# Optimization experiments

Hardware: AMD Instinct MI355X
Metric: run time of the kernel (lower is better)

The kernel has to match this reference:

```python
import jax, jax.numpy as jnp
import numpy as np

B, L, D, H = 4, 2048, 2048, 16
HD = D // H
EPS = 1e-6


def _rope_tables(l, hd, base=10000.0):
    inv = 1.0 / (base ** (np.arange(0, hd, 2, dtype=np.float32) / hd))  # [hd/2]
    t = np.arange(l, dtype=np.float32)
    ang = np.outer(t, inv)  # [l, hd/2]
    return jnp.asarray(np.cos(ang)), jnp.asarray(np.sin(ang))


def setup_inputs() -> dict:
    key = jax.random.key(0)
    ks = jax.random.split(key, 8)
    cos, sin = _rope_tables(L, HD)
    s = 1.0 / np.sqrt(D)
    return {
        "x": jax.random.normal(ks[0], (B, L, D), jnp.float32),
        "freqs_cos": cos,
        "freqs_sin": sin,
        "Wqk": jax.random.normal(ks[1], (D, 2 * D), jnp.float32) * s,
        "Wv": jax.random.normal(ks[2], (D, D), jnp.float32) * s,
        "bv": jax.random.normal(ks[3], (D,), jnp.float32) * 0.02,
        "Wp": jax.random.normal(ks[4], (D, D), jnp.float32) * s,
        "bp": jax.random.normal(ks[5], (D,), jnp.float32) * 0.02,
        "qn_w": jnp.ones((HD,), jnp.float32),
        "kn_w": jnp.ones((HD,), jnp.float32),
    }


def _rmsnorm(x, w, eps=EPS):
    ms = jnp.mean(jnp.square(x), axis=-1, keepdims=True)
    return x * jax.lax.rsqrt(ms + eps) * w


def _rope(x, cos, sin):
    # x: [b,h,l,hd]; cos/sin: [l,hd/2]; interleaved (complex) rotation
    x1 = x[..., 0::2]
    x2 = x[..., 1::2]
    c = cos[None, None, :, :]
    s = sin[None, None, :, :]
    out = jnp.stack([x1 * c - x2 * s, x1 * s + x2 * c], axis=-1)
    return out.reshape(x.shape)


def reference(x, freqs_cos, freqs_sin, Wqk, Wv, bv, Wp, bp, qn_w, kn_w):
    b, l, d = x.shape
    qk = x @ Wqk  # [b,l,2d]
    q, k = jnp.split(qk, 2, axis=-1)
    v = x @ Wv + bv
    # [b,l,d] -> [b,h,l,hd]
    to_heads = lambda t: t.reshape(b, l, H, HD).transpose(0, 2, 1, 3)
    q, k, v = to_heads(q), to_heads(k), to_heads(v)
    q = _rmsnorm(q, qn_w)
    k = _rmsnorm(k, kn_w)
    q = _rope(q, freqs_cos, freqs_sin)
    k = _rope(k, freqs_cos, freqs_sin)
    scale = 1.0 / jnp.sqrt(jnp.asarray(HD, q.dtype))
    scores = jnp.einsum("bhqd,bhkd->bhqk", q, k) * scale
    causal = jnp.tril(jnp.ones((l, l), bool))
    scores = jnp.where(causal[None, None], scores, jnp.asarray(-1e30, scores.dtype))
    attn = jax.nn.softmax(scores, axis=-1)
    y = jnp.einsum("bhqk,bhkd->bhqd", attn, v)
    y = y.transpose(0, 2, 1, 3).reshape(b, l, d)
    return y @ Wp + bp
```

## Files before the change

### kernel.cpp

```cpp
#include <hip/hip_runtime.h>
#include <hip/hip_bf16.h>
#include <math.h>

#define B_  4
#define L_  2048
#define D_  2048
#define H_  16
#define HD_ 128
#define BH_ (B_*H_)
#define BL_ (B_*L_)

typedef __attribute__((ext_vector_type(4))) float  f32x4;
typedef __attribute__((ext_vector_type(8))) __bf16 bf16x8;

static __device__ __forceinline__ float bf2f(unsigned short u) {
    union { unsigned int i; float f; } v; v.i = ((unsigned int)u) << 16; return v.f;
}
static __device__ __forceinline__ unsigned short f2bf(float f) {
    union { float f; unsigned int i; } v; v.f = f;
    unsigned int x = v.i;
    return (unsigned short)((x + 0x7fffu + ((x >> 16) & 1u)) >> 16);
}

static __device__ __forceinline__ void gload16(const unsigned short* g, unsigned short* l) {
    __builtin_amdgcn_global_load_lds(
        (const __attribute__((address_space(1))) unsigned int*)(const void*)g,
        (__attribute__((address_space(3))) unsigned int*)(void*)l, 16, 0, 0);
}

__global__ __launch_bounds__(256) void k_f32_to_bf16(const float* __restrict__ s,
                                                     unsigned short* __restrict__ d, int n8) {
    int i = blockIdx.x * 256 + threadIdx.x;
    if (i >= n8) return;
    const float* p = s + (size_t)i * 8;
    float4 a = *(const float4*)p;
    float4 b = *(const float4*)(p + 4);
    union { bf16x8 v; unsigned short u[8]; } o;
    o.u[0]=f2bf(a.x); o.u[1]=f2bf(a.y); o.u[2]=f2bf(a.z); o.u[3]=f2bf(a.w);
    o.u[4]=f2bf(b.x); o.u[5]=f2bf(b.y); o.u[6]=f2bf(b.z); o.u[7]=f2bf(b.w);
    *(bf16x8*)(d + (size_t)i * 8) = o.v;
}

__global__ __launch_bounds__(256) void k_transpose_f2b(const float* __restrict__ src,
                                                       unsigned short* __restrict__ dst,
                                                       int R, int C, int dstStride) {
    __shared__ float tile[32][33];
    int tx = threadIdx.x & 31, ty = threadIdx.x >> 5;
    int c0 = blockIdx.x * 32, r0 = blockIdx.y * 32;
    #pragma unroll
    for (int i = 0; i < 32; i += 8)
        tile[ty + i][tx] = src[(size_t)(r0 + ty + i) * C + c0 + tx];
    __syncthreads();
    #pragma unroll
    for (int i = 0; i < 32; i += 8)
        dst[(size_t)(c0 + ty + i) * dstStride + r0 + tx] = f2bf(tile[tx][ty + i]);
}


template<int MG, int NG>
static __device__ __forceinline__ void mfma_quad(const bf16x8 (&afr)[4][2],
                                                 const bf16x8 (&bfr)[2][2],
                                                 f32x4 (&acc)[8][4]) {
    #pragma unroll
    for (int mi = 0; mi < 4; ++mi)
        #pragma unroll
        for (int ni = 0; ni < 2; ++ni) {
            acc[MG*4+mi][NG*2+ni] = __builtin_amdgcn_mfma_f32_16x16x32_bf16(
                afr[mi][0], bfr[ni][0], acc[MG*4+mi][NG*2+ni], 0, 0, 0);
            acc[MG*4+mi][NG*2+ni] = __builtin_amdgcn_mfma_f32_16x16x32_bf16(
                afr[mi][1], bfr[ni][1], acc[MG*4+mi][NG*2+ni], 0, 0, 0);
        }
}

static __device__ __forceinline__ void ds_load_a(const unsigned short* u, int wm,
                                                 int l15, int l4, bf16x8 (&afr)[4][2]) {
    int sw = l15 & 7;
    #pragma unroll
    for (int mi = 0; mi < 4; ++mi) {
        int ro = (wm*64 + mi*16 + l15) * 64;
        afr[mi][0] = *(const bf16x8*)(u + ro + ((l4 ^ sw) << 3));
        afr[mi][1] = *(const bf16x8*)(u + ro + (((4 + l4) ^ sw) << 3));
    }
}

static __device__ __forceinline__ void ds_load_b(const unsigned short* u, int wn,
                                                 int l15, int l4, bf16x8 (&bfr)[2][2]) {
    int sw = l15 & 7;
    #pragma unroll
    for (int ni = 0; ni < 2; ++ni) {
        int ro = (wn*32 + ni*16 + l15) * 64;
        bfr[ni][0] = *(const bf16x8*)(u + ro + ((l4 ^ sw) << 3));
        bfr[ni][1] = *(const bf16x8*)(u + ro + (((4 + l4) ^ sw) << 3));
    }
}

#define STAGE_A_(c_, mg_, t_) do {                                                        \
    gload16(gA + (size_t)(((mg_)*64      ) * 2048) + (t_)*64, &Lds[c_][0][mg_][w*512]);   \
    gload16(gA + (size_t)(((mg_)*64 + 128) * 2048) + (t_)*64, &Lds[c_][0][mg_][4096 + w*512]); \
} while (0)
#define STAGE_B_(c_, ng_, t_) do {                                                        \
    gload16(gB + (size_t)(((ng_)*32 + ((w>>2)    )*64) * 2048) + (t_)*64, &Lds[c_][1][ng_][w*512]); \
    gload16(gB + (size_t)(((ng_)*32 + ((w>>2) + 2)*64) * 2048) + (t_)*64, &Lds[c_][1][ng_][4096 + w*512]); \
} while (0)
#define SB_() __builtin_amdgcn_sched_barrier(0)
#define READS_(c_) do {                                              \
    ds_load_a(&Lds[c_][0][0][0], wm, l15, l4, afr);  SB_();          \
    ds_load_b(&Lds[c_][1][0][0], wn, l15, l4, bf0);  SB_();          \
    ds_load_b(&Lds[c_][1][1][0], wn, l15, l4, bf1);  SB_();          \
    ds_load_a(&Lds[c_][0][1][0], wm, l15, l4, afr2); SB_();          \
} while (0)

template<int MODE>
__global__ __launch_bounds__(512, 2) void k_gemm(const unsigned short* __restrict__ A,
                                                 const unsigned short* __restrict__ Bt,
                                                 int M, int N, int K,
                                                 const float* __restrict__ bias,
                                                 unsigned short* __restrict__ qout,
                                                 unsigned short* __restrict__ kout,
                                                 unsigned short* __restrict__ vout,
                                                 float* __restrict__ fout) {
    (void)K;
    __shared__ __align__(16) unsigned short Lds[2][2][2][8192];
    const int tid = threadIdx.x;
    const int lane = tid & 63, w = tid >> 6;
    const int wm = w >> 2, wn = w & 3;
    const int l15 = lane & 15, l4 = lane >> 4;
    const int lsw = (lane & 7) ^ ((lane >> 3) & 7);

    int nwgx = gridDim.x;
    int bid = blockIdx.y * nwgx + blockIdx.x;
    int cpx = (nwgx * gridDim.y) >> 3;
    int sb = (bid & 7) * cpx + (bid >> 3);
    int n0 = (sb % nwgx) * 256, m0 = (sb / nwgx) * 256;

    const unsigned short* gA = A  + (size_t)(m0 + w*8 + (lane >> 3)) * 2048 + lsw*8;
    const unsigned short* gB = Bt + (size_t)(n0 + (w&3)*8 + (lane >> 3)) * 2048 + lsw*8;

    f32x4 acc[8][4] = {};
    bf16x8 afr[4][2], afr2[4][2], bf0[2][2], bf1[2][2];
    const int nt = 2048 / 64;

    STAGE_A_(0, 0, 0); STAGE_B_(0, 0, 0); STAGE_B_(0, 1, 0); STAGE_A_(0, 1, 0);
    STAGE_A_(1, 0, 1); STAGE_B_(1, 0, 1); STAGE_B_(1, 1, 1);
    asm volatile("s_waitcnt vmcnt(6)" ::: "memory");
    __builtin_amdgcn_s_barrier();
    READS_(0);

    for (int t = 0; t < nt; ++t) {
        const int c = t & 1, cn = c ^ 1;
        const bool h1 = (t + 1 < nt), h2 = (t + 2 < nt);

        if (h1) STAGE_A_(cn, 1, t + 1);
        __builtin_amdgcn_s_barrier();
        asm volatile("s_waitcnt lgkmcnt(12)" ::: "memory");
        SB_();
        __builtin_amdgcn_s_setprio(1);
        mfma_quad<0, 0>(afr, bf0, acc);
        __builtin_amdgcn_s_setprio(0);
        SB_();
        __builtin_amdgcn_s_barrier();

        if (h2) STAGE_A_(c, 0, t + 2);
        asm volatile("s_waitcnt lgkmcnt(8)" ::: "memory");
        SB_();
        __builtin_amdgcn_s_setprio(1);
        mfma_quad<0, 1>(afr, bf1, acc);
        __builtin_amdgcn_s_setprio(0);
        SB_();
        __builtin_amdgcn_s_barrier();

        if (h2) { STAGE_B_(c, 0, t + 2); STAGE_B_(c, 1, t + 2); }
        asm volatile("s_waitcnt lgkmcnt(0)" ::: "memory");
        SB_();
        __builtin_amdgcn_s_setprio(1);
        mfma_quad<1, 1>(afr2, bf1, acc);
        mfma_quad<1, 0>(afr2, bf0, acc);
        __builtin_amdgcn_s_setprio(0);
        SB_();
        if (h2) asm volatile("s_waitcnt vmcnt(6)" ::: "memory");
        else    asm volatile("s_waitcnt vmcnt(0)" ::: "memory");
        SB_();
        if (h1) READS_(cn);
        __builtin_amdgcn_s_barrier();
    }

    #pragma unroll
    for (int mi = 0; mi < 8; ++mi) {
        #pragma unroll
        for (int ni = 0; ni < 4; ++ni) {
            int ncol = n0 + wn*64 + ni*16 + l15;
            int mbase = m0 + wm*128 + mi*16 + l4*4;
            if (MODE == 0 && ncol >= 4096) {
                int cc = ncol - 4096, h = cc >> 7, hd = cc & 127;
                int b = mbase >> 11, l = mbase & 2047;
                float bv = bias[cc];
                ushort4 o;
                o.x = f2bf(acc[mi][ni][0] + bv);
                o.y = f2bf(acc[mi][ni][1] + bv);
                o.z = f2bf(acc[mi][ni][2] + bv);
                o.w = f2bf(acc[mi][ni][3] + bv);
                *(ushort4*)(vout + ((size_t)((b*H_ + h) * HD_ + hd)) * L_ + l) = o;
            } else {
                #pragma unroll
                for (int j = 0; j < 4; ++j) {
                    int m = mbase + j;
                    float v = acc[mi][ni][j];
                    if (MODE == 0) {
                        int b = m >> 11, l = m & 2047;
                        if (ncol < 2048) {
                            int h = ncol >> 7, hd = ncol & 127;
                            qout[((size_t)(b*H_ + h) * L_ + l) * HD_ + hd] = f2bf(v);
                        } else {
                            int cc = ncol - 2048, h = cc >> 7, hd = cc & 127;
                            kout[((size_t)(b*H_ + h) * L_ + l) * HD_ + hd] = f2bf(v);
                        }
                    } else {
                        fout[(size_t)m * N + ncol] = v + bias[ncol];
                    }
                }
            }
        }
    }
}

__global__ __launch_bounds__(256) void k_normrope(unsigned short* __restrict__ qb,
                                                  unsigned short* __restrict__ kb,
                                                  const float* __restrict__ cosT,
                                                  const float* __restrict__ sinT,
                                                  const float* __restrict__ qw,
                                                  const float* __restrict__ kw) {
    const float QSCL = 0.08838834764831845f * 1.4426950408889634f;
    int lane = threadIdx.x & 63;
    int row = blockIdx.x * 4 + (threadIdx.x >> 6);
    int isK = row >= BH_ * L_;
    unsigned short* buf = isK ? kb : qb;
    const float* w = isK ? kw : qw;
    int r = isK ? row - BH_ * L_ : row;
    int l = r & (L_ - 1);
    unsigned short* p = buf + (size_t)r * HD_ + lane * 2;
    ushort2 u = *(const ushort2*)p;
    float x1 = bf2f(u.x), x2 = bf2f(u.y);
    float ss = x1*x1 + x2*x2;
    #pragma unroll
    for (int off = 32; off; off >>= 1) ss += __shfl_xor(ss, off);
    float rs = rsqrtf(ss * (1.0f / 128.0f) + 1e-6f);
    rs *= isK ? 1.0f : QSCL;
    float c = cosT[l * 64 + lane], s = sinT[l * 64 + lane];
    float y1 = x1 * rs * w[lane * 2];
    float y2 = x2 * rs * w[lane * 2 + 1];
    ushort2 o;
    o.x = f2bf(y1 * c - y2 * s);
    o.y = f2bf(y1 * s + y2 * c);
    *(ushort2*)p = o;
}

#define PLDT 72

__global__ __launch_bounds__(256) void k_attn(const unsigned short* __restrict__ qbuf,
                                              const unsigned short* __restrict__ kbuf,
                                              const unsigned short* __restrict__ vT,
                                              unsigned short* __restrict__ yb) {
    __shared__ __align__(16) unsigned short Ks[64 * 128];
    __shared__ __align__(16) unsigned short Vs[128 * 64];
    __shared__ __align__(16) unsigned short Ps[4][32 * PLDT];
    int tid = threadIdx.x, lane = tid & 63, w = tid >> 6;
    int l15 = lane & 15, l4 = lane >> 4;
    int qb = 15 - (blockIdx.x >> 6);
    int bh = blockIdx.x & 63;
    const unsigned short* Q  = qbuf + (size_t)bh * L_ * HD_;
    const unsigned short* Kp = kbuf + (size_t)bh * L_ * HD_;
    const unsigned short* Vp = vT   + (size_t)bh * L_ * HD_;
    int qr0 = qb * 128 + w * 32;

    bf16x8 qf[2][4];
    #pragma unroll
    for (int m = 0; m < 2; ++m)
        #pragma unroll
        for (int ks = 0; ks < 4; ++ks)
            qf[m][ks] = *(const bf16x8*)(Q + (size_t)(qr0 + m*16 + l15) * HD_ + ks*32 + l4*8);

    f32x4 accO[2][8] = {};
    f32x4 accW[2] = {};

    bf16x8 vones;
    #pragma unroll
    for (int i = 0; i < 8; ++i) vones[i] = (__bf16)1.0f;

    const float BOUND = 20.0f;
    int nkt = 2 * qb + 2;

    for (int kt = 0; kt < nkt; ++kt) {
        int kbase = kt * 64;
        #pragma unroll
        for (int i = 0; i < 4; ++i) {
            int g = w * 4 + i;
            int kr = g * 4 + (lane >> 4);
            gload16(Kp + (size_t)(kbase + kr) * HD_ + (((lane & 15) ^ (kr & 15)) << 3),
                    Ks + g * 512);
            int vr = g * 8 + (lane >> 3);
            gload16(Vp + (size_t)vr * L_ + kbase + (((lane & 7) ^ (vr & 7)) << 3),
                    Vs + g * 512);
        }
        __syncthreads();

        if (kbase <= qr0 + 31) {
            f32x4 sf[2][4] = {};
            __builtin_amdgcn_s_setprio(1);
            #pragma unroll
            for (int f = 0; f < 4; ++f)
                #pragma unroll
                for (int ks = 0; ks < 4; ++ks) {
                    bf16x8 kf = *(const bf16x8*)(Ks + (f*16 + l15) * 128 +
                                                 ((((ks*4) + l4) ^ l15) << 3));
                    sf[0][f] = __builtin_amdgcn_mfma_f32_16x16x32_bf16(qf[0][ks], kf, sf[0][f], 0, 0, 0);
                    sf[1][f] = __builtin_amdgcn_mfma_f32_16x16x32_bf16(qf[1][ks], kf, sf[1][f], 0, 0, 0);
                }
            __builtin_amdgcn_s_setprio(0);

            unsigned short* ps = Ps[w];
            #pragma unroll
            for (int m = 0; m < 2; ++m) {
                bool needmask = (kbase + 63 > qr0 + m*16);
                #pragma unroll
                for (int f = 0; f < 4; ++f)
                    #pragma unroll
                    for (int j = 0; j < 4; ++j) {
                        float s = sf[m][f][j];
                        if (needmask) {
                            int key  = kbase + f*16 + l15;
                            int qrow = qr0 + m*16 + l4*4 + j;
                            if (key > qrow) s = -1e30f;
                        }
                        float p = exp2f(s - BOUND);
                        *(__bf16*)(ps + (m*16 + l4*4 + j) * PLDT + f*16 + l15) = (__bf16)p;
                    }
            }

            __builtin_amdgcn_s_setprio(1);
            #pragma unroll
            for (int ks = 0; ks < 2; ++ks) {
                bf16x8 pa0 = *(const bf16x8*)(ps + l15 * PLDT + ks*32 + l4*8);
                bf16x8 pa1 = *(const bf16x8*)(ps + (16 + l15) * PLDT + ks*32 + l4*8);
                #pragma unroll
                for (int cf = 0; cf < 8; ++cf) {
                    bf16x8 vf = *(const bf16x8*)(Vs + (cf*16 + l15) * 64 +
                                                 ((((ks*4) + l4) ^ (l15 & 7)) << 3));
                    accO[0][cf] = __builtin_amdgcn_mfma_f32_16x16x32_bf16(pa0, vf, accO[0][cf], 0, 0, 0);
                    accO[1][cf] = __builtin_amdgcn_mfma_f32_16x16x32_bf16(pa1, vf, accO[1][cf], 0, 0, 0);
                }
                accW[0] = __builtin_amdgcn_mfma_f32_16x16x32_bf16(pa0, vones, accW[0], 0, 0, 0);
                accW[1] = __builtin_amdgcn_mfma_f32_16x16x32_bf16(pa1, vones, accW[1], 0, 0, 0);
            }
            __builtin_amdgcn_s_setprio(0);
        }
        __syncthreads();
    }

    int b = bh >> 4, h = bh & 15;
    #pragma unroll
    for (int m = 0; m < 2; ++m)
        #pragma unroll
        for (int cf = 0; cf < 8; ++cf)
            #pragma unroll
            for (int j = 0; j < 4; ++j) {
                int qrow = qr0 + m*16 + l4*4 + j;
                float o = accO[m][cf][j] / accW[m][j];
                yb[((size_t)(b * L_ + qrow)) * D_ + h*128 + cf*16 + l15] = f2bf(o);
            }
}

extern "C" void kernel_launch(void* const* d_in, const int* in_sizes, int n_in,
                              void* d_out, int out_size, void* d_ws, size_t ws_size,
                              hipStream_t stream) {
    const float* x    = (const float*)d_in[0];
    const float* fcos = (const float*)d_in[1];
    const float* fsin = (const float*)d_in[2];
    const float* Wqk  = (const float*)d_in[3];
    const float* Wv   = (const float*)d_in[4];
    const float* bv   = (const float*)d_in[5];
    const float* Wp   = (const float*)d_in[6];
    const float* bp   = (const float*)d_in[7];
    const float* qn_w = (const float*)d_in[8];
    const float* kn_w = (const float*)d_in[9];
    float* out = (float*)d_out;

    char* ws = (char*)d_ws;
    unsigned short* Wt   = (unsigned short*)(ws);
    unsigned short* Wpt  = (unsigned short*)(ws + 25165824);
    unsigned short* xb   = (unsigned short*)(ws + 33554432);
    unsigned short* qbuf = (unsigned short*)(ws + 67108864);
    unsigned short* kbuf = (unsigned short*)(ws + 100663296);
    unsigned short* vTb  = (unsigned short*)(ws + 167772160);
    unsigned short* yb   = xb;

    k_f32_to_bf16<<<8192, 256, 0, stream>>>(x, xb, BL_ * D_ / 8);
    k_transpose_f2b<<<dim3(128, 64), 256, 0, stream>>>(Wqk, Wt, 2048, 4096, 2048);
    k_transpose_f2b<<<dim3(64, 64),  256, 0, stream>>>(Wv,  Wt + (size_t)4096 * 2048, 2048, 2048, 2048);
    k_transpose_f2b<<<dim3(64, 64),  256, 0, stream>>>(Wp,  Wpt, 2048, 2048, 2048);

    k_gemm<0><<<dim3(24, 32), 512, 0, stream>>>(xb, Wt, BL_, 6144, 2048, bv,
                                                qbuf, kbuf, vTb, nullptr);
    k_normrope<<<2 * BH_ * L_ / 4, 256, 0, stream>>>(qbuf, kbuf, fcos, fsin, qn_w, kn_w);
    k_attn<<<BH_ * (L_ / 128), 256, 0, stream>>>(qbuf, kbuf, vTb, yb);
    k_gemm<1><<<dim3(8, 32), 512, 0, stream>>>(yb, Wpt, BL_, 2048, 2048, bp,
                                               nullptr, nullptr, nullptr, out);
}
```

Before: 453.3 us.

## Shrink GEMM tiles to 128x128 with 4 waves and simpler double-buffered pipeline

```diff
diff --git a/kernel.cpp b/kernel.cpp
--- a/kernel.cpp
+++ b/kernel.cpp
@@ -57,61 +57,31 @@
 }
 
 
-template<int MG, int NG>
-static __device__ __forceinline__ void mfma_quad(const bf16x8 (&afr)[4][2],
-                                                 const bf16x8 (&bfr)[2][2],
-                                                 f32x4 (&acc)[8][4]) {
-    #pragma unroll
-    for (int mi = 0; mi < 4; ++mi)
-        #pragma unroll
-        for (int ni = 0; ni < 2; ++ni) {
-            acc[MG*4+mi][NG*2+ni] = __builtin_amdgcn_mfma_f32_16x16x32_bf16(
-                afr[mi][0], bfr[ni][0], acc[MG*4+mi][NG*2+ni], 0, 0, 0);
-            acc[MG*4+mi][NG*2+ni] = __builtin_amdgcn_mfma_f32_16x16x32_bf16(
-                afr[mi][1], bfr[ni][1], acc[MG*4+mi][NG*2+ni], 0, 0, 0);
-        }
-}
-
-static __device__ __forceinline__ void ds_load_a(const unsigned short* u, int wm,
-                                                 int l15, int l4, bf16x8 (&afr)[4][2]) {
+static __device__ __forceinline__ void ds_load4(const unsigned short* u, int half,
+                                                int l15, int l4, bf16x8 (&fr)[4][2]) {
     int sw = l15 & 7;
     #pragma unroll
-    for (int mi = 0; mi < 4; ++mi) {
-        int ro = (wm*64 + mi*16 + l15) * 64;
-        afr[mi][0] = *(const bf16x8*)(u + ro + ((l4 ^ sw) << 3));
-        afr[mi][1] = *(const bf16x8*)(u + ro + (((4 + l4) ^ sw) << 3));
+    for (int i = 0; i < 4; ++i) {
+        int ro = (half*64 + i*16 + l15) * 64;
+        fr[i][0] = *(const bf16x8*)(u + ro + ((l4 ^ sw) << 3));
+        fr[i][1] = *(const bf16x8*)(u + ro + (((4 + l4) ^ sw) << 3));
     }
 }
 
-static __device__ __forceinline__ void ds_load_b(const unsigned short* u, int wn,
-                                                 int l15, int l4, bf16x8 (&bfr)[2][2]) {
-    int sw = l15 & 7;
-    #pragma unroll
-    for (int ni = 0; ni < 2; ++ni) {
-        int ro = (wn*32 + ni*16 + l15) * 64;
-        bfr[ni][0] = *(const bf16x8*)(u + ro + ((l4 ^ sw) << 3));
-        bfr[ni][1] = *(const bf16x8*)(u + ro + (((4 + l4) ^ sw) << 3));
-    }
-}
-
-#define STAGE_A_(c_, mg_, t_) do {                                                        \
-    gload16(gA + (size_t)(((mg_)*64      ) * 2048) + (t_)*64, &Lds[c_][0][mg_][w*512]);   \
-    gload16(gA + (size_t)(((mg_)*64 + 128) * 2048) + (t_)*64, &Lds[c_][0][mg_][4096 + w*512]); \
+#define SB_() __builtin_amdgcn_sched_barrier(0)
+#define STAGE_T_(c_, t_) do {                                                         \
+    gload16(gA + (size_t)(0*32) * 2048 + (t_)*64, &Lds[c_][0][0*2048 + w*512]);       \
+    gload16(gB + (size_t)(0*32) * 2048 + (t_)*64, &Lds[c_][1][0*2048 + w*512]);       \
+    gload16(gA + (size_t)(1*32) * 2048 + (t_)*64, &Lds[c_][0][1*2048 + w*512]);       \
+    gload16(gB + (size_t)(1*32) * 2048 + (t_)*64, &Lds[c_][1][1*2048 + w*512]);       \
+    gload16(gA + (size_t)(2*32) * 2048 + (t_)*64, &Lds[c_][0][2*2048 + w*512]);       \
+    gload16(gB + (size_t)(2*32) * 2048 + (t_)*64, &Lds[c_][1][2*2048 + w*512]);       \
+    gload16(gA + (size_t)(3*32) * 2048 + (t_)*64, &Lds[c_][0][3*2048 + w*512]);       \
+    gload16(gB + (size_t)(3*32) * 2048 + (t_)*64, &Lds[c_][1][3*2048 + w*512]);       \
 } while (0)
-#define STAGE_B_(c_, ng_, t_) do {                                                        \
-    gload16(gB + (size_t)(((ng_)*32 + ((w>>2)    )*64) * 2048) + (t_)*64, &Lds[c_][1][ng_][w*512]); \
-    gload16(gB + (size_t)(((ng_)*32 + ((w>>2) + 2)*64) * 2048) + (t_)*64, &Lds[c_][1][ng_][4096 + w*512]); \
-} while (0)
-#define SB_() __builtin_amdgcn_sched_barrier(0)
-#define READS_(c_) do {                                              \
-    ds_load_a(&Lds[c_][0][0][0], wm, l15, l4, afr);  SB_();          \
-    ds_load_b(&Lds[c_][1][0][0], wn, l15, l4, bf0);  SB_();          \
-    ds_load_b(&Lds[c_][1][1][0], wn, l15, l4, bf1);  SB_();          \
-    ds_load_a(&Lds[c_][0][1][0], wm, l15, l4, afr2); SB_();          \
-} while (0)
 
 template<int MODE>
-__global__ __launch_bounds__(512, 2) void k_gemm(const unsigned short* __restrict__ A,
+__global__ __launch_bounds__(256, 2) void k_gemm(const unsigned short* __restrict__ A,
                                                  const unsigned short* __restrict__ Bt,
                                                  int M, int N, int K,
                                                  const float* __restrict__ bias,
@@ -120,10 +90,10 @@
                                                  unsigned short* __restrict__ vout,
                                                  float* __restrict__ fout) {
     (void)K;
-    __shared__ __align__(16) unsigned short Lds[2][2][2][8192];
+    __shared__ __align__(16) unsigned short Lds[2][2][8192];
     const int tid = threadIdx.x;
     const int lane = tid & 63, w = tid >> 6;
-    const int wm = w >> 2, wn = w & 3;
+    const int wm = w >> 1, wn = w & 1;
     const int l15 = lane & 15, l4 = lane >> 4;
     const int lsw = (lane & 7) ^ ((lane >> 3) & 7);
 
@@ -131,65 +101,59 @@
     int bid = blockIdx.y * nwgx + blockIdx.x;
     int cpx = (nwgx * gridDim.y) >> 3;
     int sb = (bid & 7) * cpx + (bid >> 3);
-    int n0 = (sb % nwgx) * 256, m0 = (sb / nwgx) * 256;
-
-    const unsigned short* gA = A  + (size_t)(m0 + w*8 + (lane >> 3)) * 2048 + lsw*8;
-    const unsigned short* gB = Bt + (size_t)(n0 + (w&3)*8 + (lane >> 3)) * 2048 + lsw*8;
-
-    f32x4 acc[8][4] = {};
-    bf16x8 afr[4][2], afr2[4][2], bf0[2][2], bf1[2][2];
+    int n0 = (sb % nwgx) * 128, m0 = (sb / nwgx) * 128;
+
+    const unsigned short* gA = A  + (size_t)(m0 + (tid >> 3)) * 2048 + lsw*8;
+    const unsigned short* gB = Bt + (size_t)(n0 + (tid >> 3)) * 2048 + lsw*8;
+
+    f32x4 acc[4][4] = {};
+    bf16x8 afr[4][2], bfr[4][2];
     const int nt = 2048 / 64;
 
-    STAGE_A_(0, 0, 0); STAGE_B_(0, 0, 0); STAGE_B_(0, 1, 0); STAGE_A_(0, 1, 0);
-    STAGE_A_(1, 0, 1); STAGE_B_(1, 0, 1); STAGE_B_(1, 1, 1);
-    asm volatile("s_waitcnt vmcnt(6)" ::: "memory");
+    STAGE_T_(0, 0);
+    STAGE_T_(1, 1);
+    asm volatile("s_waitcnt vmcnt(8)" ::: "memory");
     __builtin_amdgcn_s_barrier();
-    READS_(0);
+    ds_load4(&Lds[0][0][0], wm, l15, l4, afr);
+    ds_load4(&Lds[0][1][0], wn, l15, l4, bfr);
+    SB_();
 
     for (int t = 0; t < nt; ++t) {
         const int c = t & 1, cn = c ^ 1;
         const bool h1 = (t + 1 < nt), h2 = (t + 2 < nt);
 
-        if (h1) STAGE_A_(cn, 1, t + 1);
+        asm volatile("s_waitcnt lgkmcnt(0)" ::: "memory");
+        SB_();
         __builtin_amdgcn_s_barrier();
-        asm volatile("s_waitcnt lgkmcnt(12)" ::: "memory");
-        SB_();
+        if (h2) STAGE_T_(c, t + 2);
         __builtin_amdgcn_s_setprio(1);
-        mfma_quad<0, 0>(afr, bf0, acc);
+        #pragma unroll
+        for (int mi = 0; mi < 4; ++mi)
+            #pragma unroll
+            for (int ni = 0; ni < 4; ++ni) {
+                acc[mi][ni] = __builtin_amdgcn_mfma_f32_16x16x32_bf16(
+                    afr[mi][0], bfr[ni][0], acc[mi][ni], 0, 0, 0);
+                acc[mi][ni] = __builtin_amdgcn_mfma_f32_16x16x32_bf16(
+                    afr[mi][1], bfr[ni][1], acc[mi][ni], 0, 0, 0);
+            }
         __builtin_amdgcn_s_setprio(0);
         SB_();
+        if (h2) asm volatile("s_waitcnt vmcnt(8)" ::: "memory");
+        else    asm volatile("s_waitcnt vmcnt(0)" ::: "memory");
         __builtin_amdgcn_s_barrier();
-
-        if (h2) STAGE_A_(c, 0, t + 2);
-        asm volatile("s_waitcnt lgkmcnt(8)" ::: "memory");
-        SB_();
-        __builtin_amdgcn_s_setprio(1);
-        mfma_quad<0, 1>(afr, bf1, acc);
-        __builtin_amdgcn_s_setprio(0);
-        SB_();
-        __builtin_amdgcn_s_barrier();
-
-        if (h2) { STAGE_B_(c, 0, t + 2); STAGE_B_(c, 1, t + 2); }
-        asm volatile("s_waitcnt lgkmcnt(0)" ::: "memory");
-        SB_();
-        __builtin_amdgcn_s_setprio(1);
-        mfma_quad<1, 1>(afr2, bf1, acc);
-        mfma_quad<1, 0>(afr2, bf0, acc);
-        __builtin_amdgcn_s_setprio(0);
-        SB_();
-        if (h2) asm volatile("s_waitcnt vmcnt(6)" ::: "memory");
-        else    asm volatile("s_waitcnt vmcnt(0)" ::: "memory");
-        SB_();
-        if (h1) READS_(cn);
-        __builtin_amdgcn_s_barrier();
+        if (h1) {
+            ds_load4(&Lds[cn][0][0], wm, l15, l4, afr);
+            ds_load4(&Lds[cn][1][0], wn, l15, l4, bfr);
+            SB_();
+        }
     }
 
     #pragma unroll
-    for (int mi = 0; mi < 8; ++mi) {
+    for (int mi = 0; mi < 4; ++mi) {
         #pragma unroll
         for (int ni = 0; ni < 4; ++ni) {
             int ncol = n0 + wn*64 + ni*16 + l15;
-            int mbase = m0 + wm*128 + mi*16 + l4*4;
+            int mbase = m0 + wm*64 + mi*16 + l4*4;
             if (MODE == 0 && ncol >= 4096) {
                 int cc = ncol - 4096, h = cc >> 7, hd = cc & 127;
                 int b = mbase >> 11, l = mbase & 2047;
@@ -398,10 +362,10 @@
     k_transpose_f2b<<<dim3(64, 64),  256, 0, stream>>>(Wv,  Wt + (size_t)4096 * 2048, 2048, 2048, 2048);
     k_transpose_f2b<<<dim3(64, 64),  256, 0, stream>>>(Wp,  Wpt, 2048, 2048, 2048);
 
-    k_gemm<0><<<dim3(24, 32), 512, 0, stream>>>(xb, Wt, BL_, 6144, 2048, bv,
+    k_gemm<0><<<dim3(48, 64), 256, 0, stream>>>(xb, Wt, BL_, 6144, 2048, bv,
                                                 qbuf, kbuf, vTb, nullptr);
     k_normrope<<<2 * BH_ * L_ / 4, 256, 0, stream>>>(qbuf, kbuf, fcos, fsin, qn_w, kn_w);
     k_attn<<<BH_ * (L_ / 128), 256, 0, stream>>>(qbuf, kbuf, vTb, yb);
-    k_gemm<1><<<dim3(8, 32), 512, 0, stream>>>(yb, Wpt, BL_, 2048, 2048, bp,
-                                               nullptr, nullptr, nullptr, out);
-}
+    k_gemm<1><<<dim3(16, 64), 256, 0, stream>>>(yb, Wpt, BL_, 2048, 2048, bp,
+                                                nullptr, nullptr, nullptr, out);
+}
```

Measured after the change: 513.1 us. 1.13x slower.

## Restructure GEMM k-loop to reuse A fragment registers and unroll by two

Applied to the files above, without the earlier changes.

```diff
diff --git a/kernel.cpp b/kernel.cpp
--- a/kernel.cpp
+++ b/kernel.cpp
@@ -103,11 +103,48 @@
     gload16(gB + (size_t)(((ng_)*32 + ((w>>2) + 2)*64) * 2048) + (t_)*64, &Lds[c_][1][ng_][4096 + w*512]); \
 } while (0)
 #define SB_() __builtin_amdgcn_sched_barrier(0)
-#define READS_(c_) do {                                              \
-    ds_load_a(&Lds[c_][0][0][0], wm, l15, l4, afr);  SB_();          \
-    ds_load_b(&Lds[c_][1][0][0], wn, l15, l4, bf0);  SB_();          \
-    ds_load_b(&Lds[c_][1][1][0], wn, l15, l4, bf1);  SB_();          \
-    ds_load_a(&Lds[c_][0][1][0], wm, l15, l4, afr2); SB_();          \
+
+#define KTILE_BODY_(C_, CN_, t_) do {                                                     \
+    const bool h1 = ((t_) + 1 < nt), h2 = ((t_) + 2 < nt);                                \
+    ds_load_a(&Lds[C_][0][0][0], wm, l15, l4, afr);                                       \
+    ds_load_b(&Lds[C_][1][0][0], wn, l15, l4, bf0);                                       \
+    SB_();                                                                                \
+    ds_load_b(&Lds[C_][1][1][0], wn, l15, l4, bf1);                                       \
+    SB_();                                                                                \
+    if (h1) STAGE_A_(CN_, 1, (t_) + 1);                                                   \
+    __builtin_amdgcn_s_barrier();                                                 \
+    asm volatile("s_waitcnt lgkmcnt(4)" ::: "memory");                  \
+    SB_();                                                                                \
+    __builtin_amdgcn_s_setprio(1);                                                        \
+    mfma_quad<0, 0>(afr, bf0, acc);                                                       \
+    __builtin_amdgcn_s_setprio(0);                                                        \
+    SB_();                                                                                \
+    __builtin_amdgcn_s_barrier();                                                 \
+    asm volatile("s_waitcnt lgkmcnt(0)" ::: "memory");                     \
+    SB_();                                                                                \
+    __builtin_amdgcn_s_setprio(1);                                                        \
+    mfma_quad<0, 1>(afr, bf1, acc);                                                       \
+    __builtin_amdgcn_s_setprio(0);                                                        \
+    SB_();                                                                                \
+    ds_load_a(&Lds[C_][0][1][0], wm, l15, l4, afr);                        \
+    SB_();                                                                                \
+    if (h2) STAGE_A_(C_, 0, (t_) + 2);                                                    \
+    __builtin_amdgcn_s_barrier();                                                 \
+    if (h2) STAGE_B_(C_, 0, (t_) + 2);                                                    \
+    asm volatile("s_waitcnt lgkmcnt(0)" ::: "memory");                     \
+    SB_();                                                                                \
+    __builtin_amdgcn_s_setprio(1);                                                        \
+    mfma_quad<1, 1>(afr, bf1, acc);                                                       \
+    __builtin_amdgcn_s_setprio(0);                                                        \
+    SB_();                                                                                \
+    if (h2) STAGE_B_(C_, 1, (t_) + 2);                                                    \
+    __builtin_amdgcn_s_setprio(1);                                                        \
+    mfma_quad<1, 0>(afr, bf0, acc);                                                       \
+    __builtin_amdgcn_s_setprio(0);                                                        \
+    SB_();                                                                                \
+    if (h2) asm volatile("s_waitcnt vmcnt(6)" ::: "memory");                              \
+    else    asm volatile("s_waitcnt vmcnt(0)" ::: "memory");                              \
+    __builtin_amdgcn_s_barrier();                                                 \
 } while (0)
 
 template<int MODE>
@@ -137,51 +174,17 @@
     const unsigned short* gB = Bt + (size_t)(n0 + (w&3)*8 + (lane >> 3)) * 2048 + lsw*8;
 
     f32x4 acc[8][4] = {};
-    bf16x8 afr[4][2], afr2[4][2], bf0[2][2], bf1[2][2];
+    bf16x8 afr[4][2], bf0[2][2], bf1[2][2];
     const int nt = 2048 / 64;
 
     STAGE_A_(0, 0, 0); STAGE_B_(0, 0, 0); STAGE_B_(0, 1, 0); STAGE_A_(0, 1, 0);
     STAGE_A_(1, 0, 1); STAGE_B_(1, 0, 1); STAGE_B_(1, 1, 1);
     asm volatile("s_waitcnt vmcnt(6)" ::: "memory");
     __builtin_amdgcn_s_barrier();
-    READS_(0);
-
-    for (int t = 0; t < nt; ++t) {
-        const int c = t & 1, cn = c ^ 1;
-        const bool h1 = (t + 1 < nt), h2 = (t + 2 < nt);
-
-        if (h1) STAGE_A_(cn, 1, t + 1);
-        __builtin_amdgcn_s_barrier();
-        asm volatile("s_waitcnt lgkmcnt(12)" ::: "memory");
-        SB_();
-        __builtin_amdgcn_s_setprio(1);
-        mfma_quad<0, 0>(afr, bf0, acc);
-        __builtin_amdgcn_s_setprio(0);
-        SB_();
-        __builtin_amdgcn_s_barrier();
-
-        if (h2) STAGE_A_(c, 0, t + 2);
-        asm volatile("s_waitcnt lgkmcnt(8)" ::: "memory");
-        SB_();
-        __builtin_amdgcn_s_setprio(1);
-        mfma_quad<0, 1>(afr, bf1, acc);
-        __builtin_amdgcn_s_setprio(0);
-        SB_();
-        __builtin_amdgcn_s_barrier();
-
-        if (h2) { STAGE_B_(c, 0, t + 2); STAGE_B_(c, 1, t + 2); }
-        asm volatile("s_waitcnt lgkmcnt(0)" ::: "memory");
-        SB_();
-        __builtin_amdgcn_s_setprio(1);
-        mfma_quad<1, 1>(afr2, bf1, acc);
-        mfma_quad<1, 0>(afr2, bf0, acc);
-        __builtin_amdgcn_s_setprio(0);
-        SB_();
-        if (h2) asm volatile("s_waitcnt vmcnt(6)" ::: "memory");
-        else    asm volatile("s_waitcnt vmcnt(0)" ::: "memory");
-        SB_();
-        if (h1) READS_(cn);
-        __builtin_amdgcn_s_barrier();
+
+    for (int t = 0; t < nt; t += 2) {
+        KTILE_BODY_(0, 1, t);
+        KTILE_BODY_(1, 0, t + 1);
     }
 
     #pragma unroll
```

Measured after the change: 450.4 us. Within noise of the previous version (-0.6%).
